# Optimization experiments

Hardware: AMD Instinct MI355X
Metric: run time of the kernel (lower is better)

## Reference

```python
import jax, jax.numpy as jnp
import numpy as np

HEADS = 8
DIM_HEAD = 64
SCALE = DIM_HEAD ** (-0.5)


def setup_inputs() -> dict:
    key = jax.random.key(0)
    k1, k2, k3 = jax.random.split(key, 3)
    b, l, c = 8, 4096, 512
    x = jax.random.normal(k1, (b, l, c), dtype=jnp.float32)
    w_qkv = jax.random.normal(k2, (3 * c, c), dtype=jnp.float32) * (c ** -0.5)
    w_out = jax.random.normal(k3, (c, c), dtype=jnp.float32) * (c ** -0.5)
    b_out = jnp.zeros((c,), dtype=jnp.float32)
    return {"x": x, "w_qkv": w_qkv, "w_out": w_out, "b_out": b_out}


def reference(x, w_qkv, w_out, b_out):
    b, l, c = x.shape
    h = HEADS
    lh = l // h
    # to_qkv: Linear(dim, 3*dim, bias=False)
    qkv = x @ w_qkv.T                                   # (b, l, 3c)
    qkv = qkv.reshape(b, lh, h, 3, c).transpose(3, 0, 2, 1, 4)  # (3, b, h, l/h, c)
    q, k, v = qkv[0], qkv[1], qkv[2]                    # each (b, h, l/h, c)
    # transpose(-2,-1): attention is over the CHANNEL axis
    q = jnp.swapaxes(q, -2, -1)                         # (b, h, c, l/h)
    k = jnp.swapaxes(k, -2, -1)                         # (b, h, c, l/h)
    v = jnp.swapaxes(v, -2, -1)                         # (b, h, c, l/h)
    attn = jnp.einsum('bhcl,bhdl->bhcd', q, k) * SCALE  # (b, h, c, c)
    attn = jax.nn.softmax(attn, axis=-1)
    y = jnp.einsum('bhcd,bhdl->bhcl', attn, v)          # (b, h, c, l/h)
    y = y.transpose(0, 3, 1, 2).reshape(b, l, c)        # (b, l/h, h, c) -> (b, l, c)
    # to_out: Linear(dim, dim) + Dropout (identity at eval)
    out = y @ w_out.T + b_out
    return out
```

## Files before the change

kernel.cpp:

```cpp
#include <hip/hip_runtime.h>
#include <stdint.h>
#include <stddef.h>

typedef _Float16 f16;
typedef _Float16 f16x8 __attribute__((ext_vector_type(8)));
typedef _Float16 f16x4 __attribute__((ext_vector_type(4)));
typedef float f32x4 __attribute__((ext_vector_type(4)));

__device__ __forceinline__ void gload16(const void* g, void* l) {
    auto gp = (const __attribute__((address_space(1))) uint32_t*)(uintptr_t)g;
    auto lp = (__attribute__((address_space(3))) uint32_t*)(uintptr_t)l;
    __builtin_amdgcn_global_load_lds(gp, lp, 16, 0, 0);
}

__device__ __forceinline__ f16x4 cvt4(f32x4 v) {
    return f16x4{ (f16)v[0], (f16)v[1], (f16)v[2], (f16)v[3] };
}

__global__ __launch_bounds__(256) void prep_k(const float* __restrict__ x,
                                              const float* __restrict__ wqkv,
                                              const float* __restrict__ wout,
                                              f16* __restrict__ xb,
                                              f16* __restrict__ wqb,
                                              f16* __restrict__ wob) {
    int tid = blockIdx.x * blockDim.x + threadIdx.x;
    int stride = gridDim.x * blockDim.x;
    for (int i = tid; i < 4194304; i += stride) {
        float4 v = ((const float4*)x)[i];
        *(f16x4*)(xb + (size_t)i * 4) = f16x4{ (f16)v.x, (f16)v.y, (f16)v.z, (f16)v.w };
    }
    for (int i = tid; i < 196608; i += stride) {
        float4 v = ((const float4*)wqkv)[i];
        *(f16x4*)(wqb + (size_t)i * 4) = f16x4{ (f16)v.x, (f16)v.y, (f16)v.z, (f16)v.w };
    }
    for (int i = tid; i < 65536; i += stride) {
        float4 v = ((const float4*)wout)[i];
        *(f16x4*)(wob + (size_t)i * 4) = f16x4{ (f16)v.x, (f16)v.y, (f16)v.z, (f16)v.w };
    }
}


#define A_STAGE(NB) do {                                                        \
    gload16(Ab + kb + sE,          &ldsA[NB][( 0 + wid*8)*64]);                 \
    gload16(Ab + kb + sO + 32768,  &ldsA[NB][(32 + wid*8)*64]);                 \
    gload16(Ab + kb + sE + 65536,  &ldsA[NB][(64 + wid*8)*64]);                 \
    gload16(Ab + kb + sO + 98304,  &ldsA[NB][(96 + wid*8)*64]);                 \
    gload16(Bb + kb + sE,          &ldsB[NB][( 0 + wid*8)*64]);                 \
    gload16(Bb + kb + sO + 32768,  &ldsB[NB][(32 + wid*8)*64]);                 \
    gload16(Bb + kb + sE + 65536,  &ldsB[NB][(64 + wid*8)*64]);                 \
    gload16(Bb + kb + sO + 98304,  &ldsB[NB][(96 + wid*8)*64]);                 \
    kb += 128;                                                                  \
} while (0)

#define A_RD(SET, BUF) do {                                                     \
    _Pragma("unroll") for (int mi = 0; mi < 4; ++mi)                            \
    _Pragma("unroll") for (int kk = 0; kk < 2; ++kk)                            \
        aF##SET[mi][kk] = *(const f16x8*)(&ldsA[BUF][0] + aoff[mi][kk]);        \
    _Pragma("unroll") for (int ni = 0; ni < 4; ++ni)                            \
    _Pragma("unroll") for (int kk = 0; kk < 2; ++kk)                            \
        bF##SET[ni][kk] = *(const f16x8*)(&ldsB[BUF][0] + boff[ni][kk]);        \
} while (0)

#define A_MM(SET, KK, ML, MH_) do {                                             \
    __builtin_amdgcn_s_setprio(1);                                              \
    _Pragma("unroll") for (int mi = ML; mi < MH_; ++mi)                         \
    _Pragma("unroll") for (int ni = 0; ni < 4; ++ni) {                          \
        if constexpr (SWP)                                                      \
            acc[mi][ni] = __builtin_amdgcn_mfma_f32_16x16x32_f16(               \
                bF##SET[ni][KK], aF##SET[mi][KK], acc[mi][ni], 0, 0, 0);        \
        else                                                                    \
            acc[mi][ni] = __builtin_amdgcn_mfma_f32_16x16x32_f16(               \
                aF##SET[mi][KK], bF##SET[ni][KK], acc[mi][ni], 0, 0, 0);        \
    }                                                                           \
    __builtin_amdgcn_s_setprio(0);                                              \
} while (0)

#define A_MM3(SET)   do { A_MM(SET, 0, 0, 2); A_MM(SET, 0, 2, 4); A_MM(SET, 1, 0, 2); } while (0)
#define A_MMLAST(SET) A_MM(SET, 1, 2, 4)
#define W0  asm volatile("s_waitcnt vmcnt(0)" ::: "memory")
#define BAR __builtin_amdgcn_s_barrier()

#define A_TILE(CUR, NXT, NB, STG, FINAL) do {                                   \
    if (STG) A_STAGE(NB);                                                       \
    A_MM3(CUR);                                                                 \
    if (!FINAL) { W0; BAR; A_RD(NXT, NB); }                                     \
    A_MMLAST(CUR);                                                              \
} while (0)

template <int MODE, bool SWP, bool QK>
__global__ __launch_bounds__(256, 2) void g10_k(const f16* __restrict__ A0,
                                                const f16* __restrict__ B0,
                                                void* __restrict__ C0,
                                                void* __restrict__ C1,
                                                const float* __restrict__ bias) {
    __shared__ f16 ldsA[2][8192];
    __shared__ f16 ldsB[2][8192];

    const int tid = threadIdx.x;
    const int lane = tid & 63;
    const int wid = tid >> 6;
    const int wr = wid >> 1;
    const int wc = wid & 1;

    const int bid = blockIdx.x;
    int tm, tn;
    if constexpr (MODE == 0 && QK) {
        int swz = (bid & 7) * 256 + (bid >> 3);
        tm = (swz >> 3) * 128; tn = (swz & 7) * 128;
    } else {
        int swz = (bid & 7) * 128 + (bid >> 3);
        tm = (swz >> 2) * 128; tn = (swz & 3) * 128;
    }

    const char* Ab = (const char*)(A0 + (size_t)tm * 512);
    const char* Bb = (const char*)(B0 + (size_t)tn * 512);

    const int u = tid >> 3;
    const int colE = ((tid & 7) ^ ((u & 7) ^ (u >> 3))) * 16;
    const int sE = u * 1024 + colE;
    const int sO = sE ^ 64;
    int kb = 0;

    int aoff[4][2], boff[4][2];
#pragma unroll
    for (int mi = 0; mi < 4; ++mi) {
        int r;
        if constexpr (QK) {
            r = (lane & 15) * 8 + wr * 4 + mi;
        } else {
            r = wr * 64 + mi * 16 + (lane & 15);
        }
#pragma unroll
        for (int kk = 0; kk < 2; ++kk) {
            int c8 = (lane >> 4) + kk * 4;
            aoff[mi][kk] = r * 64 + (c8 ^ ((r & 7) ^ ((r >> 3) & 7))) * 8;
        }
    }
#pragma unroll
    for (int ni = 0; ni < 4; ++ni) {
        int r = wc * 64 + ni * 16 + (lane & 15);
#pragma unroll
        for (int kk = 0; kk < 2; ++kk) {
            int c8 = (lane >> 4) + kk * 4;
            boff[ni][kk] = r * 64 + (c8 ^ ((r & 7) ^ ((r >> 3) & 7))) * 8;
        }
    }

    f32x4 acc[4][4] = {};
    f16x8 aF0[4][2], bF0[4][2], aF1[4][2], bF1[4][2];

    A_STAGE(0);
    W0; BAR;
    A_RD(0, 0);

#pragma unroll 1
    for (int i = 0; i < 3; ++i) {
        A_TILE(0, 1, 1, true, false);
        A_TILE(1, 0, 0, true, false);
    }
    A_TILE(0, 1, 1, true, false);
    A_TILE(1, 1, 1, false, true);

    if constexpr (MODE == 0 && QK) {
        const int b = tm >> 12;
        const int lt = (tm & 4095) >> 3;
        f16* dst = (f16*)(tn < 512 ? C0 : C1);
        const int cb = (tn & 511) + wc * 64;
        const int lh0 = lt + (lane >> 4) * 4;
#pragma unroll
        for (int mi = 0; mi < 4; ++mi) {
            int h = wr * 4 + mi;
#pragma unroll
            for (int ni = 0; ni < 4; ++ni) {
                int c = cb + ni * 16 + (lane & 15);
                *(f16x4*)(dst + ((size_t)((b * 8 + h) * 512 + c)) * 512 + lh0) =
                    cvt4(acc[mi][ni]);
            }
        }
    } else {
        f16* dst = (f16*)C0;
#pragma unroll
        for (int mi = 0; mi < 4; ++mi) {
            int t = tm + wr * 64 + mi * 16 + (lane & 15);
            int b = t >> 12, l = t & 4095;
            int h = l & 7, lh = l >> 3;
#pragma unroll
            for (int ni = 0; ni < 4; ++ni) {
                int d0 = tn + wc * 64 + ni * 16 + (lane >> 4) * 4;
                *(f16x4*)(dst + ((size_t)((b * 8 + h) * 512 + lh)) * 512 + d0) =
                    cvt4(acc[mi][ni]);
            }
        }
    }
}


#define B_STAGE(NB) do {                                                        \
    gload16(At + soff,          &ldsA[NB][(  0 + wid*8)*64]);                   \
    gload16(At + soff + 65536,  &ldsA[NB][( 64 + wid*8)*64]);                   \
    gload16(At + soff + 131072, &ldsA[NB][(128 + wid*8)*64]);                   \
    gload16(At + soff + 196608, &ldsA[NB][(192 + wid*8)*64]);                   \
    gload16(Bt + soff,          &ldsB[NB][(  0 + wid*8)*64]);                   \
    gload16(Bt + soff + 65536,  &ldsB[NB][( 64 + wid*8)*64]);                   \
    gload16(Bt + soff + 131072, &ldsB[NB][(128 + wid*8)*64]);                   \
    gload16(Bt + soff + 196608, &ldsB[NB][(192 + wid*8)*64]);                   \
    At += 128; Bt += 128;                                                       \
} while (0)

#define B_RD12(KK, BUF) do {                                                    \
    _Pragma("unroll") for (int ni = 0; ni < 4; ++ni)                            \
        bF[ni] = *(const f16x8*)(&ldsB[BUF][0] + boff[ni][KK]);                 \
    _Pragma("unroll") for (int mi = 0; mi < 8; ++mi)                            \
        aF[mi] = *(const f16x8*)(&ldsA[BUF][0] + aoff[mi][KK]);                 \
} while (0)

#define B_MM32 do {                                                             \
    __builtin_amdgcn_s_setprio(1);                                              \
    _Pragma("unroll") for (int mi = 0; mi < 8; ++mi)                            \
    _Pragma("unroll") for (int ni = 0; ni < 4; ++ni) {                          \
        if constexpr (SWP)                                                      \
            acc[mi][ni] = __builtin_amdgcn_mfma_f32_16x16x32_f16(               \
                bF[ni], aF[mi], acc[mi][ni], 0, 0, 0);                          \
        else                                                                    \
            acc[mi][ni] = __builtin_amdgcn_mfma_f32_16x16x32_f16(               \
                aF[mi], bF[ni], acc[mi][ni], 0, 0, 0);                          \
    }                                                                           \
    __builtin_amdgcn_s_setprio(0);                                              \
} while (0)

#define B_TILE(CB, NB, STG, FINAL) do {                                         \
    B_RD12(0, CB);                                                              \
    if (STG) B_STAGE(NB);                                                       \
    B_MM32;                                                                     \
    B_RD12(1, CB);                                                              \
    B_MM32;                                                                     \
    if (!FINAL) { W0; BAR; }                                                    \
} while (0)

template <int MODE, bool SWP>
__global__ __launch_bounds__(512) void g12_k(const f16* __restrict__ A0,
                                             const f16* __restrict__ B0,
                                             void* __restrict__ C0,
                                             const float* __restrict__ bias) {
    __shared__ f16 ldsA[2][16384];
    __shared__ f16 ldsB[2][16384];

    const int tid = threadIdx.x;
    const int lane = tid & 63;
    const int wid = tid >> 6;
    const int wr = wid >> 2;
    const int wc = wid & 3;

    const int bid = blockIdx.x;
    int tm, tn, bh = 0;
    if constexpr (MODE == 1 || MODE == 2) {
        int swz = (bid & 7) * 32 + (bid >> 3);
        bh = swz >> 2; tm = ((swz >> 1) & 1) * 256; tn = (swz & 1) * 256;
    } else {
        int swz = (bid & 7) * 32 + (bid >> 3);
        tm = (swz >> 1) * 256; tn = (swz & 1) * 256;
    }

    const size_t bhoff = (MODE == 1 || MODE == 2) ? (size_t)bh * 262144 : 0;
    const char* At = (const char*)(A0 + bhoff + (size_t)tm * 512);
    const char* Bt = (const char*)(B0 + bhoff + (size_t)tn * 512);

    const int soff = wid * 8192 + (lane >> 3) * 1024 +
                     ((((lane & 7) ^ (lane >> 3) ^ wid) & 7) * 16);

    int aoff[8][2], boff[4][2];
#pragma unroll
    for (int mi = 0; mi < 8; ++mi) {
        int r = wr * 128 + mi * 16 + (lane & 15);
        int s3 = (r & 7) ^ ((r >> 3) & 7);
#pragma unroll
        for (int kk = 0; kk < 2; ++kk)
            aoff[mi][kk] = r * 64 + ((((lane >> 4) + kk * 4) ^ s3)) * 8;
    }
#pragma unroll
    for (int ni = 0; ni < 4; ++ni) {
        int r = wc * 64 + ni * 16 + (lane & 15);
        int s3 = (r & 7) ^ ((r >> 3) & 7);
#pragma unroll
        for (int kk = 0; kk < 2; ++kk)
            boff[ni][kk] = r * 64 + ((((lane >> 4) + kk * 4) ^ s3)) * 8;
    }

    f32x4 acc[8][4] = {};
    f16x8 aF[8], bF[4];

    B_STAGE(0);
    W0; BAR;

#pragma unroll 1
    for (int i = 0; i < 3; ++i) {
        B_TILE(0, 1, true, false);
        B_TILE(1, 0, true, false);
    }
    B_TILE(0, 1, true, false);
    B_TILE(1, 1, false, true);

    if constexpr (MODE == 1) {
        f16* S = (f16*)C0 + (size_t)bh * 262144;
#pragma unroll
        for (int mi = 0; mi < 8; ++mi) {
            int cm = tm + wr * 128 + mi * 16 + (lane & 15);
#pragma unroll
            for (int ni = 0; ni < 4; ++ni) {
                int d0 = tn + wc * 64 + ni * 16 + (lane >> 4) * 4;
                *(f16x4*)(S + (size_t)cm * 512 + d0) = cvt4(acc[mi][ni] * 0.125f);
            }
        }
    } else if constexpr (MODE == 2) {
        f16* yb = (f16*)C0;
        const int b = bh >> 3, h = bh & 7;
#pragma unroll
        for (int mi = 0; mi < 8; ++mi) {
            int c0 = tm + wr * 128 + mi * 16 + (lane >> 4) * 4;
#pragma unroll
            for (int ni = 0; ni < 4; ++ni) {
                int l = tn + wc * 64 + ni * 16 + (lane & 15);
                size_t tok = (size_t)b * 4096 + (size_t)l * 8 + h;
                *(f16x4*)(yb + tok * 512 + c0) = cvt4(acc[mi][ni]);
            }
        }
    } else {
        float* O = (float*)C0;
#pragma unroll
        for (int mi = 0; mi < 8; ++mi) {
            int m = tm + wr * 128 + mi * 16 + (lane & 15);
#pragma unroll
            for (int ni = 0; ni < 4; ++ni) {
                int n0 = tn + wc * 64 + ni * 16 + (lane >> 4) * 4;
                float4 bv = *(const float4*)(bias + n0);
                f32x4 v = acc[mi][ni];
                v[0] += bv.x; v[1] += bv.y; v[2] += bv.z; v[3] += bv.w;
                *(f32x4*)(O + (size_t)m * 512 + n0) = v;
            }
        }
    }
}

__global__ __launch_bounds__(256) void softmax_k(const f16* __restrict__ S,
                                                 f16* __restrict__ P) {
    int row = blockIdx.x * 4 + (threadIdx.x >> 6);
    int lane = threadIdx.x & 63;
    f16x8 v = *(const f16x8*)(S + (size_t)row * 512 + lane * 8);
    float f[8];
#pragma unroll
    for (int i = 0; i < 8; ++i) f[i] = (float)v[i];
    float m = f[0];
#pragma unroll
    for (int i = 1; i < 8; ++i) m = fmaxf(m, f[i]);
#pragma unroll
    for (int off = 1; off < 64; off <<= 1) m = fmaxf(m, __shfl_xor(m, off, 64));
    float s = 0.f, e[8];
#pragma unroll
    for (int i = 0; i < 8; ++i) { e[i] = __expf(f[i] - m); s += e[i]; }
#pragma unroll
    for (int off = 1; off < 64; off <<= 1) s += __shfl_xor(s, off, 64);
    float inv = 1.0f / s;
    f16x8 pk;
#pragma unroll
    for (int i = 0; i < 8; ++i) pk[i] = (f16)(e[i] * inv);
    *(f16x8*)(P + (size_t)row * 512 + lane * 8) = pk;
}

extern "C" void kernel_launch(void* const* d_in, const int* in_sizes, int n_in,
                              void* d_out, int out_size, void* d_ws, size_t ws_size,
                              hipStream_t stream) {
    const float* x = (const float*)d_in[0];
    const float* wqkv = (const float*)d_in[1];
    const float* wout = (const float*)d_in[2];
    const float* bout = (const float*)d_in[3];
    float* out = (float*)d_out;
    char* ws = (char*)d_ws;
    const size_t MBs = 1u << 20;

    f16* xb  = (f16*)(ws + 0);
    f16* wqb = (f16*)(ws + 32 * MBs);
    f16* wob = (f16*)(ws + 34 * MBs);
    f16* Qb  = (f16*)(ws + 35 * MBs);
    f16* Kb  = (f16*)(ws + 67 * MBs);
    f16* Vb  = (f16*)(ws + 99 * MBs);
    f16* Sb  = (f16*)(ws + 131 * MBs);
    f16* Pb  = xb;
    f16* yb  = Qb;

    prep_k<<<1024, 256, 0, stream>>>(x, wqkv, wout, xb, wqb, wob);
    g10_k<0, false, true><<<2048, 256, 0, stream>>>(xb, wqb, Qb, Kb, nullptr);
    g10_k<0, true, false><<<1024, 256, 0, stream>>>(xb, wqb + (size_t)1024 * 512, Vb, nullptr, nullptr);
    g12_k<1, true><<<256, 512, 0, stream>>>(Qb, Kb, Sb, nullptr);
    softmax_k<<<8192, 256, 0, stream>>>(Sb, Pb);
    g12_k<2, false><<<256, 512, 0, stream>>>(Pb, Vb, yb, nullptr);
    g12_k<3, true><<<256, 512, 0, stream>>>(yb, wob, out, bout);
}
```

Before: 191.8 us.

## Replace double-buffered QKV GEMM with single-buffer, lower-register loop

```diff
diff --git a/kernel.cpp b/kernel.cpp
--- a/kernel.cpp
+++ b/kernel.cpp
@@ -39,62 +39,50 @@
     }
 }
 
-
-#define A_STAGE(NB) do {                                                        \
-    gload16(Ab + kb + sE,          &ldsA[NB][( 0 + wid*8)*64]);                 \
-    gload16(Ab + kb + sO + 32768,  &ldsA[NB][(32 + wid*8)*64]);                 \
-    gload16(Ab + kb + sE + 65536,  &ldsA[NB][(64 + wid*8)*64]);                 \
-    gload16(Ab + kb + sO + 98304,  &ldsA[NB][(96 + wid*8)*64]);                 \
-    gload16(Bb + kb + sE,          &ldsB[NB][( 0 + wid*8)*64]);                 \
-    gload16(Bb + kb + sO + 32768,  &ldsB[NB][(32 + wid*8)*64]);                 \
-    gload16(Bb + kb + sE + 65536,  &ldsB[NB][(64 + wid*8)*64]);                 \
-    gload16(Bb + kb + sO + 98304,  &ldsB[NB][(96 + wid*8)*64]);                 \
+#define W0  asm volatile("s_waitcnt vmcnt(0)" ::: "memory")
+#define BAR __builtin_amdgcn_s_barrier()
+
+
+#define C_STAGE do {                                                            \
+    gload16(Ab + kb + sE,          &ldsA[( 0 + wid*8)*64]);                     \
+    gload16(Ab + kb + sO + 32768,  &ldsA[(32 + wid*8)*64]);                     \
+    gload16(Ab + kb + sE + 65536,  &ldsA[(64 + wid*8)*64]);                     \
+    gload16(Ab + kb + sO + 98304,  &ldsA[(96 + wid*8)*64]);                     \
+    gload16(Bb + kb + sE,          &ldsB[( 0 + wid*8)*64]);                     \
+    gload16(Bb + kb + sO + 32768,  &ldsB[(32 + wid*8)*64]);                     \
+    gload16(Bb + kb + sE + 65536,  &ldsB[(64 + wid*8)*64]);                     \
+    gload16(Bb + kb + sO + 98304,  &ldsB[(96 + wid*8)*64]);                     \
     kb += 128;                                                                  \
 } while (0)
 
-#define A_RD(SET, BUF) do {                                                     \
+#define C_RD(KK) do {                                                           \
+    _Pragma("unroll") for (int ni = 0; ni < 4; ++ni)                            \
+        bF[ni] = *(const f16x8*)(&ldsB[0] + boff[ni][KK]);                      \
     _Pragma("unroll") for (int mi = 0; mi < 4; ++mi)                            \
-    _Pragma("unroll") for (int kk = 0; kk < 2; ++kk)                            \
-        aF##SET[mi][kk] = *(const f16x8*)(&ldsA[BUF][0] + aoff[mi][kk]);        \
-    _Pragma("unroll") for (int ni = 0; ni < 4; ++ni)                            \
-    _Pragma("unroll") for (int kk = 0; kk < 2; ++kk)                            \
-        bF##SET[ni][kk] = *(const f16x8*)(&ldsB[BUF][0] + boff[ni][kk]);        \
-} while (0)
-
-#define A_MM(SET, KK, ML, MH_) do {                                             \
+        aF[mi] = *(const f16x8*)(&ldsA[0] + aoff[mi][KK]);                      \
+} while (0)
+
+#define C_MM16 do {                                                             \
     __builtin_amdgcn_s_setprio(1);                                              \
-    _Pragma("unroll") for (int mi = ML; mi < MH_; ++mi)                         \
+    _Pragma("unroll") for (int mi = 0; mi < 4; ++mi)                            \
     _Pragma("unroll") for (int ni = 0; ni < 4; ++ni) {                          \
         if constexpr (SWP)                                                      \
             acc[mi][ni] = __builtin_amdgcn_mfma_f32_16x16x32_f16(               \
-                bF##SET[ni][KK], aF##SET[mi][KK], acc[mi][ni], 0, 0, 0);        \
+                bF[ni], aF[mi], acc[mi][ni], 0, 0, 0);                          \
         else                                                                    \
             acc[mi][ni] = __builtin_amdgcn_mfma_f32_16x16x32_f16(               \
-                aF##SET[mi][KK], bF##SET[ni][KK], acc[mi][ni], 0, 0, 0);        \
+                aF[mi], bF[ni], acc[mi][ni], 0, 0, 0);                          \
     }                                                                           \
     __builtin_amdgcn_s_setprio(0);                                              \
 } while (0)
 
-#define A_MM3(SET)   do { A_MM(SET, 0, 0, 2); A_MM(SET, 0, 2, 4); A_MM(SET, 1, 0, 2); } while (0)
-#define A_MMLAST(SET) A_MM(SET, 1, 2, 4)
-#define W0  asm volatile("s_waitcnt vmcnt(0)" ::: "memory")
-#define BAR __builtin_amdgcn_s_barrier()
-
-#define A_TILE(CUR, NXT, NB, STG, FINAL) do {                                   \
-    if (STG) A_STAGE(NB);                                                       \
-    A_MM3(CUR);                                                                 \
-    if (!FINAL) { W0; BAR; A_RD(NXT, NB); }                                     \
-    A_MMLAST(CUR);                                                              \
-} while (0)
-
 template <int MODE, bool SWP, bool QK>
-__global__ __launch_bounds__(256, 2) void g10_k(const f16* __restrict__ A0,
-                                                const f16* __restrict__ B0,
-                                                void* __restrict__ C0,
-                                                void* __restrict__ C1,
-                                                const float* __restrict__ bias) {
-    __shared__ f16 ldsA[2][8192];
-    __shared__ f16 ldsB[2][8192];
+__global__ __launch_bounds__(256) void g13_k(const f16* __restrict__ A0,
+                                             const f16* __restrict__ B0,
+                                             void* __restrict__ C0,
+                                             void* __restrict__ C1) {
+    __shared__ f16 ldsA[8192];
+    __shared__ f16 ldsB[8192];
 
     const int tid = threadIdx.x;
     const int lane = tid & 63;
@@ -104,7 +92,7 @@
 
     const int bid = blockIdx.x;
     int tm, tn;
-    if constexpr (MODE == 0 && QK) {
+    if constexpr (QK) {
         int swz = (bid & 7) * 256 + (bid >> 3);
         tm = (swz >> 3) * 128; tn = (swz & 7) * 128;
     } else {
@@ -147,19 +135,18 @@
     }
 
     f32x4 acc[4][4] = {};
-    f16x8 aF0[4][2], bF0[4][2], aF1[4][2], bF1[4][2];
-
-    A_STAGE(0);
-    W0; BAR;
-    A_RD(0, 0);
+    f16x8 aF[4], bF[4];
 
 #pragma unroll 1
-    for (int i = 0; i < 3; ++i) {
-        A_TILE(0, 1, 1, true, false);
-        A_TILE(1, 0, 0, true, false);
-    }
-    A_TILE(0, 1, 1, true, false);
-    A_TILE(1, 1, 1, false, true);
+    for (int t = 0; t < 8; ++t) {
+        C_STAGE;
+        W0; BAR;
+        C_RD(0);
+        C_MM16;
+        C_RD(1);
+        C_MM16;
+        BAR;
+    }
 
     if constexpr (MODE == 0 && QK) {
         const int b = tm >> 12;
@@ -196,22 +183,22 @@
 
 
 #define B_STAGE(NB) do {                                                        \
-    gload16(At + soff,          &ldsA[NB][(  0 + wid*8)*64]);                   \
-    gload16(At + soff + 65536,  &ldsA[NB][( 64 + wid*8)*64]);                   \
-    gload16(At + soff + 131072, &ldsA[NB][(128 + wid*8)*64]);                   \
-    gload16(At + soff + 196608, &ldsA[NB][(192 + wid*8)*64]);                   \
-    gload16(Bt + soff,          &ldsB[NB][(  0 + wid*8)*64]);                   \
-    gload16(Bt + soff + 65536,  &ldsB[NB][( 64 + wid*8)*64]);                   \
-    gload16(Bt + soff + 131072, &ldsB[NB][(128 + wid*8)*64]);                   \
-    gload16(Bt + soff + 196608, &ldsB[NB][(192 + wid*8)*64]);                   \
+    gload16(At + soff,          &ldsA2[NB][(  0 + wid*8)*64]);                  \
+    gload16(At + soff + 65536,  &ldsA2[NB][( 64 + wid*8)*64]);                  \
+    gload16(At + soff + 131072, &ldsA2[NB][(128 + wid*8)*64]);                  \
+    gload16(At + soff + 196608, &ldsA2[NB][(192 + wid*8)*64]);                  \
+    gload16(Bt + soff,          &ldsB2[NB][(  0 + wid*8)*64]);                  \
+    gload16(Bt + soff + 65536,  &ldsB2[NB][( 64 + wid*8)*64]);                  \
+    gload16(Bt + soff + 131072, &ldsB2[NB][(128 + wid*8)*64]);                  \
+    gload16(Bt + soff + 196608, &ldsB2[NB][(192 + wid*8)*64]);                  \
     At += 128; Bt += 128;                                                       \
 } while (0)
 
 #define B_RD12(KK, BUF) do {                                                    \
     _Pragma("unroll") for (int ni = 0; ni < 4; ++ni)                            \
-        bF[ni] = *(const f16x8*)(&ldsB[BUF][0] + boff[ni][KK]);                 \
+        bF[ni] = *(const f16x8*)(&ldsB2[BUF][0] + boff[ni][KK]);                \
     _Pragma("unroll") for (int mi = 0; mi < 8; ++mi)                            \
-        aF[mi] = *(const f16x8*)(&ldsA[BUF][0] + aoff[mi][KK]);                 \
+        aF[mi] = *(const f16x8*)(&ldsA2[BUF][0] + aoff[mi][KK]);                \
 } while (0)
 
 #define B_MM32 do {                                                             \
@@ -242,8 +229,8 @@
                                              const f16* __restrict__ B0,
                                              void* __restrict__ C0,
                                              const float* __restrict__ bias) {
-    __shared__ f16 ldsA[2][16384];
-    __shared__ f16 ldsB[2][16384];
+    __shared__ f16 ldsA2[2][16384];
+    __shared__ f16 ldsB2[2][16384];
 
     const int tid = threadIdx.x;
     const int lane = tid & 63;
@@ -388,8 +375,8 @@
     f16* yb  = Qb;
 
     prep_k<<<1024, 256, 0, stream>>>(x, wqkv, wout, xb, wqb, wob);
-    g10_k<0, false, true><<<2048, 256, 0, stream>>>(xb, wqb, Qb, Kb, nullptr);
-    g10_k<0, true, false><<<1024, 256, 0, stream>>>(xb, wqb + (size_t)1024 * 512, Vb, nullptr, nullptr);
+    g13_k<0, false, true><<<2048, 256, 0, stream>>>(xb, wqb, Qb, Kb);
+    g13_k<0, true, false><<<1024, 256, 0, stream>>>(xb, wqb + (size_t)1024 * 512, Vb, nullptr);
     g12_k<1, true><<<256, 512, 0, stream>>>(Qb, Kb, Sb, nullptr);
     softmax_k<<<8192, 256, 0, stream>>>(Sb, Pb);
     g12_k<2, false><<<256, 512, 0, stream>>>(Pb, Vb, yb, nullptr);
```

After: 198.2 us. 3.3% more time.

## Fuse QK^T score GEMM with row softmax in one kernel

Applied to the files above, without the earlier changes.

```diff
diff --git a/kernel.cpp b/kernel.cpp
--- a/kernel.cpp
+++ b/kernel.cpp
@@ -38,6 +38,9 @@
         *(f16x4*)(wob + (size_t)i * 4) = f16x4{ (f16)v.x, (f16)v.y, (f16)v.z, (f16)v.w };
     }
 }
+
+#define W0  asm volatile("s_waitcnt vmcnt(0)" ::: "memory")
+#define BAR __builtin_amdgcn_s_barrier()
 
 
 #define A_STAGE(NB) do {                                                        \
@@ -77,8 +80,6 @@
 
 #define A_MM3(SET)   do { A_MM(SET, 0, 0, 2); A_MM(SET, 0, 2, 4); A_MM(SET, 1, 0, 2); } while (0)
 #define A_MMLAST(SET) A_MM(SET, 1, 2, 4)
-#define W0  asm volatile("s_waitcnt vmcnt(0)" ::: "memory")
-#define BAR __builtin_amdgcn_s_barrier()
 
 #define A_TILE(CUR, NXT, NB, STG, FINAL) do {                                   \
     if (STG) A_STAGE(NB);                                                       \
@@ -195,23 +196,174 @@
 }
 
 
+#define S_STAGE do {                                                            \
+    gload16(Qt + kb + soff,           &ldsA[(  0 + wid*8)*64]);                 \
+    gload16(Qt + kb + soff + 65536,   &ldsA[( 64 + wid*8)*64]);                 \
+    gload16(Kt + kb + soff,           &ldsB[(  0 + wid*8)*64]);                 \
+    gload16(Kt + kb + soff + 65536,   &ldsB[( 64 + wid*8)*64]);                 \
+    gload16(Kt + kb + soff + 131072,  &ldsB[(128 + wid*8)*64]);                 \
+    gload16(Kt + kb + soff + 196608,  &ldsB[(192 + wid*8)*64]);                 \
+    gload16(Kt + kb + soff + 262144,  &ldsB[(256 + wid*8)*64]);                 \
+    gload16(Kt + kb + soff + 327680,  &ldsB[(320 + wid*8)*64]);                 \
+    gload16(Kt + kb + soff + 393216,  &ldsB[(384 + wid*8)*64]);                 \
+    gload16(Kt + kb + soff + 458752,  &ldsB[(448 + wid*8)*64]);                 \
+    kb += 128;                                                                  \
+} while (0)
+
+#define S_RD(KK) do {                                                           \
+    _Pragma("unroll") for (int ni = 0; ni < 4; ++ni)                            \
+        bF[ni] = *(const f16x8*)(&ldsB[0] + boff[ni][KK]);                      \
+    _Pragma("unroll") for (int mi = 0; mi < 8; ++mi)                            \
+        aF[mi] = *(const f16x8*)(&ldsA[0] + aoff[mi][KK]);                      \
+} while (0)
+
+#define S_MM do {                                                               \
+    __builtin_amdgcn_s_setprio(1);                                              \
+    _Pragma("unroll") for (int mi = 0; mi < 8; ++mi)                            \
+    _Pragma("unroll") for (int ni = 0; ni < 4; ++ni)                            \
+        acc[mi][ni] = __builtin_amdgcn_mfma_f32_16x16x32_f16(                   \
+            aF[mi], bF[ni], acc[mi][ni], 0, 0, 0);                              \
+    __builtin_amdgcn_s_setprio(0);                                              \
+} while (0)
+
+__global__ __launch_bounds__(512) void sfm_k(const f16* __restrict__ Qb,
+                                             const f16* __restrict__ Kb,
+                                             f16* __restrict__ Pb) {
+    __shared__ f16 ldsA[128 * 64];
+    __shared__ f16 ldsB[512 * 64];
+    __shared__ float red[8 * 128];
+    __shared__ float redg[128];
+
+    const int tid = threadIdx.x;
+    const int lane = tid & 63;
+    const int wid = tid >> 6;
+    const int g = lane >> 4;
+    const int li = lane & 15;
+
+    const int bid = blockIdx.x;
+    const int swz = (bid & 7) * 32 + (bid >> 3);
+    const int bh = swz >> 2, ct = swz & 3;
+
+    const char* Qt = (const char*)(Qb + (size_t)bh * 262144 + (size_t)ct * 128 * 512);
+    const char* Kt = (const char*)(Kb + (size_t)bh * 262144);
+
+    const int soff = (tid >> 3) * 1024 +
+                     ((((lane & 7) ^ (lane >> 3) ^ wid) & 7) * 16);
+    int kb = 0;
+
+    int aoff[8][2], boff[4][2];
+#pragma unroll
+    for (int mi = 0; mi < 8; ++mi) {
+        int r = mi * 16 + li;
+        int s3 = (r & 7) ^ ((r >> 3) & 7);
+#pragma unroll
+        for (int kk = 0; kk < 2; ++kk)
+            aoff[mi][kk] = r * 64 + (((g + kk * 4) ^ s3)) * 8;
+    }
+#pragma unroll
+    for (int ni = 0; ni < 4; ++ni) {
+        int r = wid * 64 + ni * 16 + li;
+        int s3 = (r & 7) ^ ((r >> 3) & 7);
+#pragma unroll
+        for (int kk = 0; kk < 2; ++kk)
+            boff[ni][kk] = r * 64 + (((g + kk * 4) ^ s3)) * 8;
+    }
+
+    f32x4 acc[8][4] = {};
+    f16x8 aF[8], bF[4];
+
+#pragma unroll 1
+    for (int t = 0; t < 8; ++t) {
+        S_STAGE;
+        W0; BAR;
+        S_RD(0);
+        S_MM;
+        S_RD(1);
+        S_MM;
+        BAR;
+    }
+
+#pragma unroll
+    for (int mi = 0; mi < 8; ++mi)
+#pragma unroll
+        for (int ni = 0; ni < 4; ++ni) acc[mi][ni] *= 0.125f;
+
+#pragma unroll
+    for (int mi = 0; mi < 8; ++mi)
+#pragma unroll
+        for (int j = 0; j < 4; ++j) {
+            float v = fmaxf(fmaxf(acc[mi][0][j], acc[mi][1][j]),
+                            fmaxf(acc[mi][2][j], acc[mi][3][j]));
+#pragma unroll
+            for (int off = 1; off < 16; off <<= 1) v = fmaxf(v, __shfl_xor(v, off, 64));
+            if (li == 0) red[wid * 128 + mi * 16 + g * 4 + j] = v;
+        }
+    BAR;
+    if (tid < 128) {
+        float m = red[tid];
+#pragma unroll
+        for (int w = 1; w < 8; ++w) m = fmaxf(m, red[w * 128 + tid]);
+        redg[tid] = m;
+    }
+    BAR;
+
+#pragma unroll
+    for (int mi = 0; mi < 8; ++mi)
+#pragma unroll
+        for (int j = 0; j < 4; ++j) {
+            float mg = redg[mi * 16 + g * 4 + j];
+            float s = 0.f;
+#pragma unroll
+            for (int ni = 0; ni < 4; ++ni) {
+                float e = __expf(acc[mi][ni][j] - mg);
+                acc[mi][ni][j] = e;
+                s += e;
+            }
+#pragma unroll
+            for (int off = 1; off < 16; off <<= 1) s += __shfl_xor(s, off, 64);
+            if (li == 0) red[wid * 128 + mi * 16 + g * 4 + j] = s;
+        }
+    BAR;
+    if (tid < 128) {
+        float s = red[tid];
+#pragma unroll
+        for (int w = 1; w < 8; ++w) s += red[w * 128 + tid];
+        redg[tid] = 1.0f / s;
+    }
+    BAR;
+
+    f16* Pt = Pb + (size_t)bh * 262144;
+#pragma unroll
+    for (int mi = 0; mi < 8; ++mi)
+#pragma unroll
+        for (int j = 0; j < 4; ++j) {
+            int row = mi * 16 + g * 4 + j;
+            float is = redg[row];
+            size_t base = (size_t)(ct * 128 + row) * 512 + wid * 64 + li;
+#pragma unroll
+            for (int ni = 0; ni < 4; ++ni)
+                Pt[base + ni * 16] = (f16)(acc[mi][ni][j] * is);
+        }
+}
+
+
 #define B_STAGE(NB) do {                                                        \
-    gload16(At + soff,          &ldsA[NB][(  0 + wid*8)*64]);                   \
-    gload16(At + soff + 65536,  &ldsA[NB][( 64 + wid*8)*64]);                   \
-    gload16(At + soff + 131072, &ldsA[NB][(128 + wid*8)*64]);                   \
-    gload16(At + soff + 196608, &ldsA[NB][(192 + wid*8)*64]);                   \
-    gload16(Bt + soff,          &ldsB[NB][(  0 + wid*8)*64]);                   \
-    gload16(Bt + soff + 65536,  &ldsB[NB][( 64 + wid*8)*64]);                   \
-    gload16(Bt + soff + 131072, &ldsB[NB][(128 + wid*8)*64]);                   \
-    gload16(Bt + soff + 196608, &ldsB[NB][(192 + wid*8)*64]);                   \
+    gload16(At + soff,          &ldsA2[NB][(  0 + wid*8)*64]);                  \
+    gload16(At + soff + 65536,  &ldsA2[NB][( 64 + wid*8)*64]);                  \
+    gload16(At + soff + 131072, &ldsA2[NB][(128 + wid*8)*64]);                  \
+    gload16(At + soff + 196608, &ldsA2[NB][(192 + wid*8)*64]);                  \
+    gload16(Bt + soff,          &ldsB2[NB][(  0 + wid*8)*64]);                  \
+    gload16(Bt + soff + 65536,  &ldsB2[NB][( 64 + wid*8)*64]);                  \
+    gload16(Bt + soff + 131072, &ldsB2[NB][(128 + wid*8)*64]);                  \
+    gload16(Bt + soff + 196608, &ldsB2[NB][(192 + wid*8)*64]);                  \
     At += 128; Bt += 128;                                                       \
 } while (0)
 
 #define B_RD12(KK, BUF) do {                                                    \
     _Pragma("unroll") for (int ni = 0; ni < 4; ++ni)                            \
-        bF[ni] = *(const f16x8*)(&ldsB[BUF][0] + boff[ni][KK]);                 \
+        bF[ni] = *(const f16x8*)(&ldsB2[BUF][0] + boff[ni][KK]);                \
     _Pragma("unroll") for (int mi = 0; mi < 8; ++mi)                            \
-        aF[mi] = *(const f16x8*)(&ldsA[BUF][0] + aoff[mi][KK]);                 \
+        aF[mi] = *(const f16x8*)(&ldsA2[BUF][0] + aoff[mi][KK]);                \
 } while (0)
 
 #define B_MM32 do {                                                             \
@@ -242,8 +394,8 @@
                                              const f16* __restrict__ B0,
                                              void* __restrict__ C0,
                                              const float* __restrict__ bias) {
-    __shared__ f16 ldsA[2][16384];
-    __shared__ f16 ldsB[2][16384];
+    __shared__ f16 ldsA2[2][16384];
+    __shared__ f16 ldsB2[2][16384];
 
     const int tid = threadIdx.x;
     const int lane = tid & 63;
@@ -253,7 +405,7 @@
 
     const int bid = blockIdx.x;
     int tm, tn, bh = 0;
-    if constexpr (MODE == 1 || MODE == 2) {
+    if constexpr (MODE == 2) {
         int swz = (bid & 7) * 32 + (bid >> 3);
         bh = swz >> 2; tm = ((swz >> 1) & 1) * 256; tn = (swz & 1) * 256;
     } else {
@@ -261,7 +413,7 @@
         tm = (swz >> 1) * 256; tn = (swz & 1) * 256;
     }
 
-    const size_t bhoff = (MODE == 1 || MODE == 2) ? (size_t)bh * 262144 : 0;
+    const size_t bhoff = (MODE == 2) ? (size_t)bh * 262144 : 0;
     const char* At = (const char*)(A0 + bhoff + (size_t)tm * 512);
     const char* Bt = (const char*)(B0 + bhoff + (size_t)tn * 512);
 
@@ -300,18 +452,7 @@
     B_TILE(0, 1, true, false);
     B_TILE(1, 1, false, true);
 
-    if constexpr (MODE == 1) {
-        f16* S = (f16*)C0 + (size_t)bh * 262144;
-#pragma unroll
-        for (int mi = 0; mi < 8; ++mi) {
-            int cm = tm + wr * 128 + mi * 16 + (lane & 15);
-#pragma unroll
-            for (int ni = 0; ni < 4; ++ni) {
-                int d0 = tn + wc * 64 + ni * 16 + (lane >> 4) * 4;
-                *(f16x4*)(S + (size_t)cm * 512 + d0) = cvt4(acc[mi][ni] * 0.125f);
-            }
-        }
-    } else if constexpr (MODE == 2) {
+    if constexpr (MODE == 2) {
         f16* yb = (f16*)C0;
         const int b = bh >> 3, h = bh & 7;
 #pragma unroll
@@ -339,31 +480,6 @@
             }
         }
     }
-}
-
-__global__ __launch_bounds__(256) void softmax_k(const f16* __restrict__ S,
-                                                 f16* __restrict__ P) {
-    int row = blockIdx.x * 4 + (threadIdx.x >> 6);
-    int lane = threadIdx.x & 63;
-    f16x8 v = *(const f16x8*)(S + (size_t)row * 512 + lane * 8);
-    float f[8];
-#pragma unroll
-    for (int i = 0; i < 8; ++i) f[i] = (float)v[i];
-    float m = f[0];
-#pragma unroll
-    for (int i = 1; i < 8; ++i) m = fmaxf(m, f[i]);
-#pragma unroll
-    for (int off = 1; off < 64; off <<= 1) m = fmaxf(m, __shfl_xor(m, off, 64));
-    float s = 0.f, e[8];
-#pragma unroll
-    for (int i = 0; i < 8; ++i) { e[i] = __expf(f[i] - m); s += e[i]; }
-#pragma unroll
-    for (int off = 1; off < 64; off <<= 1) s += __shfl_xor(s, off, 64);
-    float inv = 1.0f / s;
-    f16x8 pk;
-#pragma unroll
-    for (int i = 0; i < 8; ++i) pk[i] = (f16)(e[i] * inv);
-    *(f16x8*)(P + (size_t)row * 512 + lane * 8) = pk;
 }
 
 extern "C" void kernel_launch(void* const* d_in, const int* in_sizes, int n_in,
@@ -383,15 +499,13 @@
     f16* Qb  = (f16*)(ws + 35 * MBs);
     f16* Kb  = (f16*)(ws + 67 * MBs);
     f16* Vb  = (f16*)(ws + 99 * MBs);
-    f16* Sb  = (f16*)(ws + 131 * MBs);
     f16* Pb  = xb;
     f16* yb  = Qb;
 
     prep_k<<<1024, 256, 0, stream>>>(x, wqkv, wout, xb, wqb, wob);
     g10_k<0, false, true><<<2048, 256, 0, stream>>>(xb, wqb, Qb, Kb, nullptr);
     g10_k<0, true, false><<<1024, 256, 0, stream>>>(xb, wqb + (size_t)1024 * 512, Vb, nullptr, nullptr);
-    g12_k<1, true><<<256, 512, 0, stream>>>(Qb, Kb, Sb, nullptr);
-    softmax_k<<<8192, 256, 0, stream>>>(Sb, Pb);
+    sfm_k<<<256, 512, 0, stream>>>(Qb, Kb, Pb);
     g12_k<2, false><<<256, 512, 0, stream>>>(Pb, Vb, yb, nullptr);
     g12_k<3, true><<<256, 512, 0, stream>>>(yb, wob, out, bout);
 }
```

Result: no change. 193.2 us (+0.7%).
